# Performance work log

Measured on AMD Instinct MI355X. Metric: run time of the kernel, lower is better.

The kernel has to match this reference:

```python
import jax, jax.numpy as jnp
import numpy as np

N = 20000        # nodes
E = 160000       # directed edges (before self loops)
NODE_DIM = 1287
HEADS = 4
C1, C2, C3 = 128, 256, 128
ACT_SLOPE = 0.15   # module's LeakyReLU between layers
GAT_SLOPE = 0.2    # PyG GATConv default negative_slope


def _gat_layer(x, src, dst, W, att_src, att_dst, bias, heads, out_dim, concat):
    # x: [N, in] ; W: [in, heads*out] ; att_*: [heads, out] ; bias: [heads*out] or [out]
    h = (x @ W).reshape(N, heads, out_dim)                      # [N, H, C]
    a_s = jnp.einsum('nhc,hc->nh', h, att_src)                  # [N, H]
    a_d = jnp.einsum('nhc,hc->nh', h, att_dst)                  # [N, H]
    e = jax.nn.leaky_relu(a_s[src] + a_d[dst], GAT_SLOPE)       # [Etot, H]
    # segment softmax over incoming edges of each dst node (self loops => no empty segments)
    m = jax.ops.segment_max(e, dst, num_segments=N)             # [N, H]
    w = jnp.exp(e - m[dst])
    den = jax.ops.segment_sum(w, dst, num_segments=N)           # [N, H]
    alpha = w / den[dst]                                        # [Etot, H]
    msg = h[src] * alpha[:, :, None]                            # [Etot, H, C]
    out = jax.ops.segment_sum(msg, dst, num_segments=N)         # [N, H, C]
    out = out.reshape(N, heads * out_dim) if concat else out.mean(axis=1)
    return out + bias


def setup_inputs() -> dict:
    key = jax.random.key(0)
    ks = jax.random.split(key, 22)
    s = 0.05
    x = jax.random.normal(ks[0], (N, NODE_DIM), jnp.float32)
    edge_index = jax.random.randint(ks[1], (2, E), 0, N, dtype=jnp.int64)
    inp = {
        'x': x, 'edge_index': edge_index,
        'W1': jax.random.normal(ks[2], (NODE_DIM, HEADS * C1), jnp.float32) * s,
        'as1': jax.random.normal(ks[3], (HEADS, C1), jnp.float32) * s,
        'ad1': jax.random.normal(ks[4], (HEADS, C1), jnp.float32) * s,
        'b1': jnp.zeros((HEADS * C1,), jnp.float32),
        'W2': jax.random.normal(ks[5], (HEADS * C1, HEADS * C2), jnp.float32) * s,
        'as2': jax.random.normal(ks[6], (HEADS, C2), jnp.float32) * s,
        'ad2': jax.random.normal(ks[7], (HEADS, C2), jnp.float32) * s,
        'b2': jnp.zeros((HEADS * C2,), jnp.float32),
        # conv3: 1024 -> 128, 1 head, no concat
        'W3': jax.random.normal(ks[8], (HEADS * C2, C3), jnp.float32) * s,
        'as3': jax.random.normal(ks[9], (1, C3), jnp.float32) * s,
        'ad3': jax.random.normal(ks[10], (1, C3), jnp.float32) * s,
        'b3': jnp.zeros((C3,), jnp.float32),
        # pre_fc: 128 -> 16
        'pw': jax.random.normal(ks[11], (C3, 16), jnp.float32) * s,
        'pb': jnp.zeros((16,), jnp.float32),
        # fc fallback: Linear(16,32) -> LeakyReLU(0.15) -> Linear(32,2)
        'f1w': jax.random.normal(ks[12], (16, 32), jnp.float32) * s,
        'f1b': jnp.zeros((32,), jnp.float32),
        'f2w': jax.random.normal(ks[13], (32, 2), jnp.float32) * s,
        'f2b': jnp.zeros((2,), jnp.float32),
    }
    return inp


def reference(x, edge_index, W1, as1, ad1, b1, W2, as2, ad2, b2,
              W3, as3, ad3, b3, pw, pb, f1w, f1b, f2w, f2b):
    loop = jnp.arange(N, dtype=edge_index.dtype)
    src = jnp.concatenate([edge_index[0], loop])   # PyG add_self_loops=True
    dst = jnp.concatenate([edge_index[1], loop])
    h = _gat_layer(x, src, dst, W1, as1, ad1, b1, HEADS, C1, True)
    h = jax.nn.leaky_relu(h, ACT_SLOPE)            # dropout = identity (eval)
    h = _gat_layer(h, src, dst, W2, as2, ad2, b2, HEADS, C2, True)
    h = jax.nn.leaky_relu(h, ACT_SLOPE)
    h = _gat_layer(h, src, dst, W3, as3, ad3, b3, 1, C3, False)
    h = jax.nn.leaky_relu(h, ACT_SLOPE)
    h = h @ pw + pb                                 # pre_fc (128 -> 16)
    h = jax.nn.leaky_relu(h @ f1w + f1b, ACT_SLOPE)
    return h @ f2w + f2b                            # [N, 2] logits
```

## Files before the change

kernel.cpp:

```cpp
#include <hip/hip_runtime.h>
#include <hip/hip_bf16.h>
#include <cstdint>
#include <cstddef>

#define LRELU(x, s) ((x) > 0.f ? (x) : (s) * (x))

typedef __attribute__((ext_vector_type(8))) short bf16x8;
typedef __attribute__((ext_vector_type(4))) float f32x4;

__device__ __forceinline__ float bflo(uint v) { return __uint_as_float(v << 16); }
__device__ __forceinline__ float bfhi(uint v) { return __uint_as_float(v & 0xffff0000u); }
__device__ __forceinline__ ushort f2bf(float f) {
  const uint u = __float_as_uint(f);
  return (ushort)((u + 0x7fffu + ((u >> 16) & 1u)) >> 16);
}
__device__ __forceinline__ float rl_f(float x, int j) {
  return __uint_as_float(__builtin_amdgcn_readlane(__float_as_uint(x), j));
}

__device__ __forceinline__ void async16(const ushort* g, ushort* l) {
  __builtin_amdgcn_global_load_lds(
      (const __attribute__((address_space(1))) unsigned int*)g,
      (__attribute__((address_space(3))) unsigned int*)l, 16, 0, 0);
}

#define WAITCNT_VM(n) (0xF70 | (n))

__global__ void cast_pad_rows(const float* __restrict__ in, ushort* __restrict__ out,
                              int rows, int K, int Kp) {
  const int P4 = Kp >> 2;
  const long long idx = (long long)blockIdx.x * blockDim.x + threadIdx.x;
  if (idx >= (long long)rows * P4) return;
  const int r = (int)(idx / P4);
  const int c = ((int)(idx - (long long)r * P4)) << 2;
  const float* p = in + (size_t)r * K + c;
  float v0 = 0.f, v1 = 0.f, v2 = 0.f, v3 = 0.f;
  if (c + 3 < K) { v0 = p[0]; v1 = p[1]; v2 = p[2]; v3 = p[3]; }
  else {
    if (c + 0 < K) v0 = p[0];
    if (c + 1 < K) v1 = p[1];
    if (c + 2 < K) v2 = p[2];
    if (c + 3 < K) v3 = p[3];
  }
  uint2 o;
  o.x = (uint)f2bf(v0) | ((uint)f2bf(v1) << 16);
  o.y = (uint)f2bf(v2) | ((uint)f2bf(v3) << 16);
  *(uint2*)(out + (size_t)r * Kp + c) = o;
}

__global__ void cast_W_T(const float* __restrict__ W, ushort* __restrict__ Wt,
                         int K, int Nn, int Kp) {
  __shared__ float tile[32][33];
  const int kt = blockIdx.x * 32;
  const int nt = blockIdx.y * 32;
  const int tx = threadIdx.x;
  const int ty = threadIdx.y;
  for (int r = ty; r < 32; r += 8) {
    const int k = kt + r, nn = nt + tx;
    tile[r][tx] = (k < K && nn < Nn) ? W[(size_t)k * Nn + nn] : 0.f;
  }
  __syncthreads();
  for (int r = ty; r < 32; r += 8) {
    const int nn = nt + r, k = kt + tx;
    if (nn < Nn && k < Kp) Wt[(size_t)nn * Kp + k] = f2bf(tile[tx][r]);
  }
}

template <int TM, int TAG>
__global__ __launch_bounds__(256) void gemm_bf16(
    const ushort* __restrict__ A, const ushort* __restrict__ Bt, ushort* __restrict__ C,
    int M, int N, int Kp) {
  constexpr int MI = TM / 32;
  constexpr int LPG = (TM == 128) ? 4 : 3;
  __shared__ ushort sA[2 * TM * 32];
  __shared__ ushort sB[2 * 128 * 32];
  const int tid = threadIdx.x;
  const int wave = tid >> 6;
  const int lane = tid & 63;
  const int tilesN = N >> 7;
  const int nwg = gridDim.x;
  const int q8 = nwg >> 3, r8 = nwg & 7;
  const int xcd = blockIdx.x & 7;
  const int lid = blockIdx.x >> 3;
  const int wg = (xcd < r8 ? xcd * (q8 + 1) : r8 * (q8 + 1) + (xcd - r8) * q8) + lid;
  const int bx = wg % tilesN;
  const int by = wg / tilesN;
  const int wrow = (wave >> 1) * (TM / 2);
  const int wcol = (wave & 1) * 64;
  const int quad = lane >> 4;
  const int ml = lane & 15;

  const int seg = (((lane & 3) ^ ((lane >> 3) & 3)) * 8);
  const int rB0 = wave * 32 + (lane >> 2);
  const int gB0 = bx * 128 + rB0;
  const ushort* pB0 = Bt + (size_t)gB0 * Kp + seg;
  const ushort* pB1 = Bt + (size_t)(gB0 + 16) * Kp + seg;
  ushort* lB0 = &sB[(wave * 32) * 32];
  ushort* lB1 = &sB[(wave * 32 + 16) * 32];
  const ushort *pA0, *pA1;
  ushort *lA0, *lA1;
  if constexpr (TM == 128) {
    const int r0 = wave * 32 + (lane >> 2);
    pA0 = A + (size_t)min(by * TM + r0, M - 1) * Kp + seg;
    pA1 = A + (size_t)min(by * TM + r0 + 16, M - 1) * Kp + seg;
    lA0 = &sA[(wave * 32) * 32];
    lA1 = &sA[(wave * 32 + 16) * 32];
  } else {
    const int r0 = wave * 16 + (lane >> 2);
    pA0 = A + (size_t)min(by * TM + r0, M - 1) * Kp + seg;
    pA1 = nullptr;
    lA0 = &sA[(wave * 16) * 32];
    lA1 = nullptr;
  }

  const int nIter = Kp >> 5;
  auto issue = [&](int it, int p) {
    const int k0 = it << 5;
    const int oa = p * TM * 32;
    const int ob_ = p * 128 * 32;
    async16(pA0 + k0, lA0 + oa);
    if constexpr (TM == 128) async16(pA1 + k0, lA1 + oa);
    async16(pB0 + k0, lB0 + ob_);
    async16(pB1 + k0, lB1 + ob_);
  };

  f32x4 acc[MI][4];
#pragma unroll
  for (int mi = 0; mi < MI; mi++)
#pragma unroll
    for (int ni = 0; ni < 4; ni++)
#pragma unroll
      for (int e = 0; e < 4; e++) acc[mi][ni][e] = 0.f;

  const int rq = (quad ^ ((ml >> 1) & 3)) * 8;

  issue(0, 0);
  if (nIter > 1) issue(1, 1);
  int p = 0;
  for (int it = 0; it < nIter; ++it) {
    if (it + 1 < nIter) __builtin_amdgcn_s_waitcnt(WAITCNT_VM(LPG));
    else __builtin_amdgcn_s_waitcnt(WAITCNT_VM(0));
    __builtin_amdgcn_s_barrier();
    const ushort* bA = &sA[p * TM * 32];
    const ushort* bB = &sB[p * 128 * 32];
    bf16x8 af[MI], bfr[4];
#pragma unroll
    for (int mi = 0; mi < MI; mi++)
      af[mi] = *(const bf16x8*)&bA[(wrow + mi * 16 + ml) * 32 + rq];
#pragma unroll
    for (int ni = 0; ni < 4; ni++)
      bfr[ni] = *(const bf16x8*)&bB[(wcol + ni * 16 + ml) * 32 + rq];
#pragma unroll
    for (int mi = 0; mi < MI; mi++)
#pragma unroll
      for (int ni = 0; ni < 4; ni++)
        acc[mi][ni] = __builtin_amdgcn_mfma_f32_16x16x32_bf16(af[mi], bfr[ni], acc[mi][ni], 0, 0, 0);
    if (it + 2 < nIter) {
      __builtin_amdgcn_s_barrier();
      issue(it + 2, p);
    }
    p ^= 1;
  }

#pragma unroll
  for (int mi = 0; mi < MI; mi++) {
#pragma unroll
    for (int r = 0; r < 4; r++) {
      const int row = by * TM + wrow + mi * 16 + quad * 4 + r;
      if (row < M) {
#pragma unroll
        for (int ni = 0; ni < 4; ni++) {
          const int col = bx * 128 + wcol + ni * 16 + ml;
          C[(size_t)row * N + col] = f2bf(acc[mi][ni][r]);
        }
      }
    }
  }
}

template <int H, int C>
__global__ __launch_bounds__(256) void att_dots(
    const ushort* __restrict__ hb, const float* __restrict__ AS,
    const float* __restrict__ AD, float* __restrict__ asb, float* __restrict__ adb,
    int Nn) {
  constexpr int HC = H * C;
  constexpr int EPL = HC / 64;
  constexpr int S = C / EPL;
  const int n = blockIdx.x * 4 + (threadIdx.x >> 6);
  const int lane = threadIdx.x & 63;
  if (n >= Nn) return;
  const int head = lane / S;
  const int cbase = (lane % S) * EPL;
  const ushort* row = hb + (size_t)n * HC + lane * EPL;
  const float* as_h = AS + head * C;
  const float* ad_h = AD + head * C;
  float ps = 0.f, pd = 0.f;
#pragma unroll
  for (int j = 0; j < EPL; j += 2) {
    const uint v = *(const uint*)(row + j);
    const float lo = bflo(v), hi = bfhi(v);
    ps += lo * as_h[cbase + j] + hi * as_h[cbase + j + 1];
    pd += lo * ad_h[cbase + j] + hi * ad_h[cbase + j + 1];
  }
#pragma unroll
  for (int off = 1; off < S; off <<= 1) {
    ps += __shfl_xor(ps, off);
    pd += __shfl_xor(pd, off);
  }
  if ((lane % S) == 0) {
    asb[n * H + head] = ps;
    adb[n * H + head] = pd;
  }
}

__global__ void count_deg(const int* __restrict__ dst, int E, int* __restrict__ deg) {
  const int t = blockIdx.x * blockDim.x + threadIdx.x;
  if (t < E) atomicAdd(&deg[dst[t]], 1);
}

__global__ __launch_bounds__(1024) void scan_kernel(const int* __restrict__ deg,
                                                    int* __restrict__ rowptr,
                                                    int* __restrict__ cursor, int n) {
  __shared__ int swsum[16];
  __shared__ int carry_s;
  const int t = threadIdx.x;
  const int wv = t >> 6, lane = t & 63;
  if (t == 0) carry_s = 0;
  __syncthreads();
  for (int base = 0; base < n; base += 1024) {
    const int i = base + t;
    const int v = (i < n) ? (deg[i] + 1) : 0;
    int sc = v;
#pragma unroll
    for (int off = 1; off < 64; off <<= 1) {
      const int u = __shfl_up(sc, off);
      if (lane >= off) sc += u;
    }
    if (lane == 63) swsum[wv] = sc;
    __syncthreads();
    if (t < 16) {
      int x = swsum[t];
#pragma unroll
      for (int off = 1; off < 16; off <<= 1) {
        const int u = __shfl_up(x, off);
        if (t >= off) x += u;
      }
      swsum[t] = x;
    }
    __syncthreads();
    const int incl = sc + (wv == 0 ? 0 : swsum[wv - 1]) + carry_s;
    if (i < n) { rowptr[i + 1] = incl; cursor[i] = incl - v; }
    if (base == 0 && t == 0) rowptr[0] = 0;
    __syncthreads();
    if (t == 0) carry_s += swsum[15];
    __syncthreads();
  }
}

__global__ void scatter_edges(const int* __restrict__ esrc, const int* __restrict__ edst,
                              int E, int Etot, int* __restrict__ cursor,
                              int* __restrict__ csr_src) {
  const int t = blockIdx.x * blockDim.x + threadIdx.x;
  if (t >= Etot) return;
  int s, d;
  if (t < E) { s = esrc[t]; d = edst[t]; } else { s = t - E; d = s; }
  const int pos = atomicAdd(&cursor[d], 1);
  csr_src[pos] = s;
}

template <int H, int C>
__global__ __launch_bounds__(256) void gat_agg_wave(
    const ushort* __restrict__ hb, const int* __restrict__ rowptr,
    const int* __restrict__ csr_src, const float* __restrict__ a_s,
    const float* __restrict__ a_d, const float* __restrict__ bias,
    ushort* __restrict__ outb, float act_slope, int Nn) {
  constexpr int HC = H * C;
  constexpr int NU = HC / 2;
  constexpr int UPT = NU / 256;
  constexpr int GRP = (UPT == 2) ? 4 : 8;
  const int n = blockIdx.x * 4 + (threadIdx.x >> 6);
  const int lane = threadIdx.x & 63;
  if (n >= Nn) return;
  float ad_n[H];
#pragma unroll
  for (int h = 0; h < H; h++) ad_n[h] = a_d[n * H + h];
  const int start = rowptr[n], end = rowptr[n + 1];
  f32x4 acc[UPT][2];
#pragma unroll
  for (int q = 0; q < UPT; q++)
#pragma unroll
    for (int u = 0; u < 2; u++)
#pragma unroll
      for (int e = 0; e < 4; e++) acc[q][u][e] = 0.f;
  float den[H];
#pragma unroll
  for (int h = 0; h < H; h++) den[h] = 0.f;

  for (int base = start; base < end; base += 64) {
    const int cnt = min(64, end - base);
    int s = 0;
    float w[H];
#pragma unroll
    for (int h = 0; h < H; h++) w[h] = 0.f;
    if (lane < cnt) {
      s = csr_src[base + lane];
      float asv[H];
      if constexpr (H == 4) {
        const float4 t4 = *(const float4*)(a_s + s * 4);
        asv[0] = t4.x; asv[1] = t4.y; asv[2] = t4.z; asv[3] = t4.w;
      } else {
        asv[0] = a_s[s];
      }
#pragma unroll
      for (int h = 0; h < H; h++) {
        float lg = asv[h] + ad_n[h];
        lg = LRELU(lg, 0.2f);
        w[h] = __expf(lg);
        den[h] += w[h];
      }
    }
    const int cntg = cnt & ~(GRP - 1);
    int j = 0;
    for (; j < cntg; j += GRP) {
      uint4 v[GRP][UPT];
#pragma unroll
      for (int g = 0; g < GRP; g++) {
        const int sj = __builtin_amdgcn_readlane(s, j + g);
        const uint4* hp = (const uint4*)(hb + (size_t)sj * HC);
#pragma unroll
        for (int q = 0; q < UPT; q++) v[g][q] = hp[q * 64 + lane];
      }
#pragma unroll
      for (int g = 0; g < GRP; g++) {
        float wj[H];
#pragma unroll
        for (int h = 0; h < H; h++) wj[h] = rl_f(w[h], j + g);
#pragma unroll
        for (int q = 0; q < UPT; q++) {
          const int e0 = q * 512 + 8 * lane;
          const float wq = wj[e0 / C];
          acc[q][0][0] += wq * bflo(v[g][q].x);
          acc[q][0][1] += wq * bfhi(v[g][q].x);
          acc[q][0][2] += wq * bflo(v[g][q].y);
          acc[q][0][3] += wq * bfhi(v[g][q].y);
          acc[q][1][0] += wq * bflo(v[g][q].z);
          acc[q][1][1] += wq * bfhi(v[g][q].z);
          acc[q][1][2] += wq * bflo(v[g][q].w);
          acc[q][1][3] += wq * bfhi(v[g][q].w);
        }
      }
    }
    for (; j < cnt; j++) {
      const int sj = __builtin_amdgcn_readlane(s, j);
      float wj[H];
#pragma unroll
      for (int h = 0; h < H; h++) wj[h] = rl_f(w[h], j);
      const uint4* hp = (const uint4*)(hb + (size_t)sj * HC);
#pragma unroll
      for (int q = 0; q < UPT; q++) {
        const int e0 = q * 512 + 8 * lane;
        const uint4 v = hp[q * 64 + lane];
        const float wq = wj[e0 / C];
        acc[q][0][0] += wq * bflo(v.x);
        acc[q][0][1] += wq * bfhi(v.x);
        acc[q][0][2] += wq * bflo(v.y);
        acc[q][0][3] += wq * bfhi(v.y);
        acc[q][1][0] += wq * bflo(v.z);
        acc[q][1][1] += wq * bfhi(v.z);
        acc[q][1][2] += wq * bflo(v.w);
        acc[q][1][3] += wq * bfhi(v.w);
      }
    }
  }
#pragma unroll
  for (int h = 0; h < H; h++) {
#pragma unroll
    for (int off = 1; off < 64; off <<= 1) den[h] += __shfl_xor(den[h], off);
    den[h] = 1.f / den[h];
  }
#pragma unroll
  for (int q = 0; q < UPT; q++) {
    const int e0 = q * 512 + 8 * lane;
    const float iv = den[e0 / C];
    const float4 ba = *(const float4*)(bias + e0);
    const float4 bb = *(const float4*)(bias + e0 + 4);
    const float o0 = LRELU(acc[q][0][0] * iv + ba.x, act_slope);
    const float o1 = LRELU(acc[q][0][1] * iv + ba.y, act_slope);
    const float o2 = LRELU(acc[q][0][2] * iv + ba.z, act_slope);
    const float o3 = LRELU(acc[q][0][3] * iv + ba.w, act_slope);
    const float o4 = LRELU(acc[q][1][0] * iv + bb.x, act_slope);
    const float o5 = LRELU(acc[q][1][1] * iv + bb.y, act_slope);
    const float o6 = LRELU(acc[q][1][2] * iv + bb.z, act_slope);
    const float o7 = LRELU(acc[q][1][3] * iv + bb.w, act_slope);
    uint4 o;
    o.x = (uint)f2bf(o0) | ((uint)f2bf(o1) << 16);
    o.y = (uint)f2bf(o2) | ((uint)f2bf(o3) << 16);
    o.z = (uint)f2bf(o4) | ((uint)f2bf(o5) << 16);
    o.w = (uint)f2bf(o6) | ((uint)f2bf(o7) << 16);
    ((uint4*)outb)[(size_t)n * (NU / 4) + q * 64 + lane] = o;
  }
}

__global__ __launch_bounds__(64) void gat_agg3_mlp(
    const ushort* __restrict__ hb, const int* __restrict__ rowptr,
    const int* __restrict__ csr_src, const float* __restrict__ a_s,
    const float* __restrict__ a_d, const float* __restrict__ b3,
    const float* __restrict__ pw, const float* __restrict__ pb,
    const float* __restrict__ f1w, const float* __restrict__ f1b,
    const float* __restrict__ f2w, const float* __restrict__ f2b,
    float* __restrict__ out) {
  const int n = blockIdx.x;
  const int tid = threadIdx.x;
  __shared__ float sx[128];
  __shared__ float s1[16];
  __shared__ float s2[32];
  const float ad_n = a_d[n];
  const int start = rowptr[n], end = rowptr[n + 1];
  float2 acc = make_float2(0.f, 0.f);
  float den = 0.f;
  for (int base = start; base < end; base += 64) {
    const int cnt = min(64, end - base);
    int s = 0;
    float w = 0.f;
    if (tid < cnt) {
      s = csr_src[base + tid];
      float lg = a_s[s] + ad_n;
      lg = LRELU(lg, 0.2f);
      w = __expf(lg);
      den += w;
    }
    const int cntg = cnt & ~7;
    int j = 0;
    for (; j < cntg; j += 8) {
      uint v[8];
      float wj[8];
#pragma unroll
      for (int g = 0; g < 8; g++) {
        const int sj = __builtin_amdgcn_readlane(s, j + g);
        v[g] = ((const uint*)(hb + (size_t)sj * 128))[tid];
        wj[g] = rl_f(w, j + g);
      }
#pragma unroll
      for (int g = 0; g < 8; g++) {
        acc.x += wj[g] * bflo(v[g]);
        acc.y += wj[g] * bfhi(v[g]);
      }
    }
    for (; j < cnt; j++) {
      const int sj = __builtin_amdgcn_readlane(s, j);
      const float wj = rl_f(w, j);
      const uint v = ((const uint*)(hb + (size_t)sj * 128))[tid];
      acc.x += wj * bflo(v);
      acc.y += wj * bfhi(v);
    }
  }
#pragma unroll
  for (int off = 1; off < 64; off <<= 1) den += __shfl_xor(den, off);
  const float iv = 1.f / den;
  sx[2 * tid]     = LRELU(acc.x * iv + b3[2 * tid], 0.15f);
  sx[2 * tid + 1] = LRELU(acc.y * iv + b3[2 * tid + 1], 0.15f);
  __syncthreads();
  if (tid < 16) {
    float a = pb[tid];
    for (int c = 0; c < 128; c++) a += sx[c] * pw[c * 16 + tid];
    s1[tid] = a;
  }
  __syncthreads();
  if (tid < 32) {
    float a = f1b[tid];
    for (int c = 0; c < 16; c++) a += s1[c] * f1w[c * 32 + tid];
    s2[tid] = LRELU(a, 0.15f);
  }
  __syncthreads();
  if (tid < 2) {
    float a = f2b[tid];
    for (int c = 0; c < 32; c++) a += s2[c] * f2w[c * 2 + tid];
    out[(size_t)n * 2 + tid] = a;
  }
}

extern "C" void kernel_launch(void* const* d_in, const int* in_sizes, int n_in,
                              void* d_out, int out_size, void* d_ws, size_t ws_size,
                              hipStream_t stream) {
  const float* x   = (const float*)d_in[0];
  const int* ei    = (const int*)d_in[1];
  const float* W1  = (const float*)d_in[2];
  const float* as1 = (const float*)d_in[3];
  const float* ad1 = (const float*)d_in[4];
  const float* b1  = (const float*)d_in[5];
  const float* W2  = (const float*)d_in[6];
  const float* as2 = (const float*)d_in[7];
  const float* ad2 = (const float*)d_in[8];
  const float* b2  = (const float*)d_in[9];
  const float* W3  = (const float*)d_in[10];
  const float* as3 = (const float*)d_in[11];
  const float* ad3 = (const float*)d_in[12];
  const float* b3  = (const float*)d_in[13];
  const float* pw  = (const float*)d_in[14];
  const float* pb  = (const float*)d_in[15];
  const float* f1w = (const float*)d_in[16];
  const float* f1b = (const float*)d_in[17];
  const float* f2w = (const float*)d_in[18];
  const float* f2b = (const float*)d_in[19];
  float* out = (float*)d_out;

  const int N = in_sizes[0] / 1287;
  const int E = in_sizes[1] / 2;
  const int Etot = E + N;
  const int* esrc = ei;
  const int* edst = ei + E;
  const int K1 = 1287, K1p = 1312;

  char* ws = (char*)d_ws;
  size_t off = 0;
  auto alloc = [&](size_t bytes) -> void* {
    void* p = ws + off;
    off = (off + bytes + 255) & ~(size_t)255;
    return p;
  };
  ushort* hb  = (ushort*)alloc((size_t)N * 1024 * 2);
  ushort* ob  = (ushort*)alloc((size_t)N * 1024 * 2);
  ushort* xb  = (ushort*)alloc((size_t)N * K1p * 2);
  ushort* W1t = (ushort*)alloc((size_t)512 * K1p * 2);
  ushort* W2t = (ushort*)alloc((size_t)1024 * 512 * 2);
  ushort* W3t = (ushort*)alloc((size_t)128 * 1024 * 2);
  float* av   = (float*)alloc((size_t)N * 8 * sizeof(float));
  int* deg    = (int*)alloc((size_t)N * sizeof(int));
  int* rowptr = (int*)alloc((size_t)(N + 1) * sizeof(int));
  int* cursor = (int*)alloc((size_t)N * sizeof(int));
  int* csr    = (int*)alloc((size_t)Etot * sizeof(int));
  float* asb = av;
  float* adb = av + (size_t)N * 4;

  hipMemsetAsync(deg, 0, (size_t)N * sizeof(int), stream);
  count_deg<<<(E + 255) / 256, 256, 0, stream>>>(edst, E, deg);
  scan_kernel<<<1, 1024, 0, stream>>>(deg, rowptr, cursor, N);
  scatter_edges<<<(Etot + 255) / 256, 256, 0, stream>>>(esrc, edst, E, Etot, cursor, csr);

  {
    const long long nx = (long long)N * (K1p / 4);
    cast_pad_rows<<<(int)((nx + 255) / 256), 256, 0, stream>>>(x, xb, N, K1, K1p);
    cast_W_T<<<dim3(K1p / 32, (512 + 31) / 32), dim3(32, 8), 0, stream>>>(W1, W1t, K1, 512, K1p);
    cast_W_T<<<dim3(512 / 32, 1024 / 32), dim3(32, 8), 0, stream>>>(W2, W2t, 512, 1024, 512);
    cast_W_T<<<dim3(1024 / 32, 128 / 32), dim3(32, 8), 0, stream>>>(W3, W3t, 1024, 128, 1024);
  }

  const int tilesM = (N + 127) / 128;
  const int tilesM64 = (N + 63) / 64;
  const int nodeBlocks = (N + 3) / 4;

  {
    const int HC = 512;
    gemm_bf16<128, 1><<<tilesM * (HC / 128), 256, 0, stream>>>(xb, W1t, hb, N, HC, K1p);
    att_dots<4, 128><<<nodeBlocks, 256, 0, stream>>>(hb, as1, ad1, asb, adb, N);
    gat_agg_wave<4, 128><<<nodeBlocks, 256, 0, stream>>>(hb, rowptr, csr, asb, adb,
                                                         b1, ob, 0.15f, N);
  }
  {
    const int HC = 1024;
    gemm_bf16<128, 2><<<tilesM * (HC / 128), 256, 0, stream>>>(ob, W2t, hb, N, HC, 512);
    att_dots<4, 256><<<nodeBlocks, 256, 0, stream>>>(hb, as2, ad2, asb, adb, N);
    gat_agg_wave<4, 256><<<nodeBlocks, 256, 0, stream>>>(hb, rowptr, csr, asb, adb,
                                                         b2, ob, 0.15f, N);
  }
  {
    const int HC = 128;
    gemm_bf16<64, 3><<<tilesM64 * (HC / 128), 256, 0, stream>>>(ob, W3t, hb, N, HC, 1024);
    att_dots<1, 128><<<nodeBlocks, 256, 0, stream>>>(hb, as3, ad3, asb, adb, N);
    gat_agg3_mlp<<<N, 64, 0, stream>>>(hb, rowptr, csr, asb, adb, b3,
                                       pw, pb, f1w, f1b, f2w, f2b, out);
  }
}
```

Baseline: 479.5 us.

## Fuse prep kernels, triple-buffer GEMM loads, batch layer-3 aggregation per wave

Merges the x cast, the three weight transposes and the degree memset into one `prep_all` launch, replacing several launches and a memset. The bf16 GEMM moves from double to triple LDS buffering, so the next-but-one tile load is issued right after the single barrier. This drops the second barrier per K step, at the cost of more shared memory per block. The final aggregation+MLP kernel now handles four nodes per 256-thread block, one per wave, and computes the small MLP with lane-parallel partial dots and shuffle reductions instead of serial single-thread loops and block barriers.

Result: faster. 455.4 us (-5.0%).

```diff
diff --git a/kernel.cpp b/kernel.cpp
--- a/kernel.cpp
+++ b/kernel.cpp
@@ -26,35 +26,51 @@
 
 #define WAITCNT_VM(n) (0xF70 | (n))
 
-__global__ void cast_pad_rows(const float* __restrict__ in, ushort* __restrict__ out,
-                              int rows, int K, int Kp) {
-  const int P4 = Kp >> 2;
-  const long long idx = (long long)blockIdx.x * blockDim.x + threadIdx.x;
-  if (idx >= (long long)rows * P4) return;
-  const int r = (int)(idx / P4);
-  const int c = ((int)(idx - (long long)r * P4)) << 2;
-  const float* p = in + (size_t)r * K + c;
-  float v0 = 0.f, v1 = 0.f, v2 = 0.f, v3 = 0.f;
-  if (c + 3 < K) { v0 = p[0]; v1 = p[1]; v2 = p[2]; v3 = p[3]; }
+__global__ __launch_bounds__(256) void prep_all(
+    const float* __restrict__ x, ushort* __restrict__ xb,
+    const float* __restrict__ W1, ushort* __restrict__ W1t,
+    const float* __restrict__ W2, ushort* __restrict__ W2t,
+    const float* __restrict__ W3, ushort* __restrict__ W3t,
+    int* __restrict__ deg,
+    int N, int K1, int K1p, int nA, int nB, int nC, int nD) {
+  __shared__ float tile[32][33];
+  const int tid = threadIdx.x;
+  int b = blockIdx.x;
+  if (b < nA) {
+    const int P4 = K1p >> 2;
+    const long long idx = (long long)b * 256 + tid;
+    if (idx < (long long)N * P4) {
+      const int r = (int)(idx / P4);
+      const int c = ((int)(idx - (long long)r * P4)) << 2;
+      const float* p = x + (size_t)r * K1 + c;
+      float v0 = 0.f, v1 = 0.f, v2 = 0.f, v3 = 0.f;
+      if (c + 3 < K1) { v0 = p[0]; v1 = p[1]; v2 = p[2]; v3 = p[3]; }
+      else {
+        if (c + 0 < K1) v0 = p[0];
+        if (c + 1 < K1) v1 = p[1];
+        if (c + 2 < K1) v2 = p[2];
+        if (c + 3 < K1) v3 = p[3];
+      }
+      uint2 o;
+      o.x = (uint)f2bf(v0) | ((uint)f2bf(v1) << 16);
+      o.y = (uint)f2bf(v2) | ((uint)f2bf(v3) << 16);
+      *(uint2*)(xb + (size_t)r * K1p + c) = o;
+    }
+    return;
+  }
+  b -= nA;
+  const float* W; ushort* Wt; int K, Nn, Kp, tilesK;
+  if (b < nB)           { W = W1; Wt = W1t; K = K1;   Nn = 512;  Kp = K1p;  tilesK = K1p / 32; }
+  else if (b < nB + nC) { b -= nB; W = W2; Wt = W2t; K = 512;  Nn = 1024; Kp = 512;  tilesK = 16; }
+  else if (b < nB + nC + nD) { b -= nB + nC; W = W3; Wt = W3t; K = 1024; Nn = 128; Kp = 1024; tilesK = 32; }
   else {
-    if (c + 0 < K) v0 = p[0];
-    if (c + 1 < K) v1 = p[1];
-    if (c + 2 < K) v2 = p[2];
-    if (c + 3 < K) v3 = p[3];
-  }
-  uint2 o;
-  o.x = (uint)f2bf(v0) | ((uint)f2bf(v1) << 16);
-  o.y = (uint)f2bf(v2) | ((uint)f2bf(v3) << 16);
-  *(uint2*)(out + (size_t)r * Kp + c) = o;
-}
-
-__global__ void cast_W_T(const float* __restrict__ W, ushort* __restrict__ Wt,
-                         int K, int Nn, int Kp) {
-  __shared__ float tile[32][33];
-  const int kt = blockIdx.x * 32;
-  const int nt = blockIdx.y * 32;
-  const int tx = threadIdx.x;
-  const int ty = threadIdx.y;
+    const int i = (b - nB - nC - nD) * 256 + tid;
+    if (i < N) deg[i] = 0;
+    return;
+  }
+  const int kt = (b % tilesK) * 32;
+  const int nt = (b / tilesK) * 32;
+  const int tx = tid & 31, ty = tid >> 5;
   for (int r = ty; r < 32; r += 8) {
     const int k = kt + r, nn = nt + tx;
     tile[r][tx] = (k < K && nn < Nn) ? W[(size_t)k * Nn + nn] : 0.f;
@@ -72,8 +88,8 @@
     int M, int N, int Kp) {
   constexpr int MI = TM / 32;
   constexpr int LPG = (TM == 128) ? 4 : 3;
-  __shared__ ushort sA[2 * TM * 32];
-  __shared__ ushort sB[2 * 128 * 32];
+  __shared__ ushort sA[3 * TM * 32];
+  __shared__ ushort sB[3 * 128 * 32];
   const int tid = threadIdx.x;
   const int wave = tid >> 6;
   const int lane = tid & 63;
@@ -136,13 +152,17 @@
 
   issue(0, 0);
   if (nIter > 1) issue(1, 1);
-  int p = 0;
+  int b = 0;
   for (int it = 0; it < nIter; ++it) {
     if (it + 1 < nIter) __builtin_amdgcn_s_waitcnt(WAITCNT_VM(LPG));
     else __builtin_amdgcn_s_waitcnt(WAITCNT_VM(0));
     __builtin_amdgcn_s_barrier();
-    const ushort* bA = &sA[p * TM * 32];
-    const ushort* bB = &sB[p * 128 * 32];
+    if (it + 2 < nIter) {
+      const int b2 = (b + 2 >= 3) ? b - 1 : b + 2;
+      issue(it + 2, b2);
+    }
+    const ushort* bA = &sA[b * TM * 32];
+    const ushort* bB = &sB[b * 128 * 32];
     bf16x8 af[MI], bfr[4];
 #pragma unroll
     for (int mi = 0; mi < MI; mi++)
@@ -155,11 +175,7 @@
 #pragma unroll
       for (int ni = 0; ni < 4; ni++)
         acc[mi][ni] = __builtin_amdgcn_mfma_f32_16x16x32_bf16(af[mi], bfr[ni], acc[mi][ni], 0, 0, 0);
-    if (it + 2 < nIter) {
-      __builtin_amdgcn_s_barrier();
-      issue(it + 2, p);
-    }
-    p ^= 1;
+    b = (b + 1 == 3) ? 0 : b + 1;
   }
 
 #pragma unroll
@@ -401,19 +417,21 @@
   }
 }
 
-__global__ __launch_bounds__(64) void gat_agg3_mlp(
+__global__ __launch_bounds__(256) void gat_agg3_mlp(
     const ushort* __restrict__ hb, const int* __restrict__ rowptr,
     const int* __restrict__ csr_src, const float* __restrict__ a_s,
     const float* __restrict__ a_d, const float* __restrict__ b3,
     const float* __restrict__ pw, const float* __restrict__ pb,
     const float* __restrict__ f1w, const float* __restrict__ f1b,
     const float* __restrict__ f2w, const float* __restrict__ f2b,
-    float* __restrict__ out) {
-  const int n = blockIdx.x;
-  const int tid = threadIdx.x;
-  __shared__ float sx[128];
-  __shared__ float s1[16];
-  __shared__ float s2[32];
+    float* __restrict__ out, int Nn) {
+  __shared__ float sx[4][128];
+  __shared__ float s1[4][16];
+  __shared__ float s2[4][32];
+  const int w = threadIdx.x >> 6;
+  const int lane = threadIdx.x & 63;
+  const int n = blockIdx.x * 4 + w;
+  if (n >= Nn) return;
   const float ad_n = a_d[n];
   const int start = rowptr[n], end = rowptr[n + 1];
   float2 acc = make_float2(0.f, 0.f);
@@ -421,13 +439,13 @@
   for (int base = start; base < end; base += 64) {
     const int cnt = min(64, end - base);
     int s = 0;
-    float w = 0.f;
-    if (tid < cnt) {
-      s = csr_src[base + tid];
+    float wv_ = 0.f;
+    if (lane < cnt) {
+      s = csr_src[base + lane];
       float lg = a_s[s] + ad_n;
       lg = LRELU(lg, 0.2f);
-      w = __expf(lg);
-      den += w;
+      wv_ = __expf(lg);
+      den += wv_;
     }
     const int cntg = cnt & ~7;
     int j = 0;
@@ -437,8 +455,8 @@
 #pragma unroll
       for (int g = 0; g < 8; g++) {
         const int sj = __builtin_amdgcn_readlane(s, j + g);
-        v[g] = ((const uint*)(hb + (size_t)sj * 128))[tid];
-        wj[g] = rl_f(w, j + g);
+        v[g] = ((const uint*)(hb + (size_t)sj * 128))[lane];
+        wj[g] = rl_f(wv_, j + g);
       }
 #pragma unroll
       for (int g = 0; g < 8; g++) {
@@ -448,8 +466,8 @@
     }
     for (; j < cnt; j++) {
       const int sj = __builtin_amdgcn_readlane(s, j);
-      const float wj = rl_f(w, j);
-      const uint v = ((const uint*)(hb + (size_t)sj * 128))[tid];
+      const float wj = rl_f(wv_, j);
+      const uint v = ((const uint*)(hb + (size_t)sj * 128))[lane];
       acc.x += wj * bflo(v);
       acc.y += wj * bfhi(v);
     }
@@ -457,25 +475,34 @@
 #pragma unroll
   for (int off = 1; off < 64; off <<= 1) den += __shfl_xor(den, off);
   const float iv = 1.f / den;
-  sx[2 * tid]     = LRELU(acc.x * iv + b3[2 * tid], 0.15f);
-  sx[2 * tid + 1] = LRELU(acc.y * iv + b3[2 * tid + 1], 0.15f);
-  __syncthreads();
-  if (tid < 16) {
-    float a = pb[tid];
-    for (int c = 0; c < 128; c++) a += sx[c] * pw[c * 16 + tid];
-    s1[tid] = a;
-  }
-  __syncthreads();
-  if (tid < 32) {
-    float a = f1b[tid];
-    for (int c = 0; c < 16; c++) a += s1[c] * f1w[c * 32 + tid];
-    s2[tid] = LRELU(a, 0.15f);
-  }
-  __syncthreads();
-  if (tid < 2) {
-    float a = f2b[tid];
-    for (int c = 0; c < 32; c++) a += s2[c] * f2w[c * 2 + tid];
-    out[(size_t)n * 2 + tid] = a;
+  sx[w][2 * lane]     = LRELU(acc.x * iv + b3[2 * lane], 0.15f);
+  sx[w][2 * lane + 1] = LRELU(acc.y * iv + b3[2 * lane + 1], 0.15f);
+  {
+    const int o = lane & 15, p = lane >> 4;
+    float a = 0.f;
+#pragma unroll
+    for (int c = 0; c < 32; c++) a += sx[w][p * 32 + c] * pw[(p * 32 + c) * 16 + o];
+    a += __shfl_xor(a, 16);
+    a += __shfl_xor(a, 32);
+    if (lane < 16) s1[w][o] = a + pb[o];
+  }
+  {
+    const int o = lane & 31, p = lane >> 5;
+    float a = 0.f;
+#pragma unroll
+    for (int c = 0; c < 8; c++) a += s1[w][p * 8 + c] * f1w[(p * 8 + c) * 32 + o];
+    a += __shfl_xor(a, 32);
+    if (lane < 32) s2[w][o] = LRELU(a + f1b[o], 0.15f);
+  }
+  {
+    const int o = lane & 1, p = lane >> 1;
+    float a = s2[w][p] * f2w[p * 2 + o];
+    a += __shfl_xor(a, 2);
+    a += __shfl_xor(a, 4);
+    a += __shfl_xor(a, 8);
+    a += __shfl_xor(a, 16);
+    a += __shfl_xor(a, 32);
+    if (lane < 2) out[(size_t)n * 2 + o] = a + f2b[o];
   }
 }
 
@@ -532,18 +559,17 @@
   float* asb = av;
   float* adb = av + (size_t)N * 4;
 
-  hipMemsetAsync(deg, 0, (size_t)N * sizeof(int), stream);
+  const int nA = (int)(((long long)N * (K1p / 4) + 255) / 256);
+  const int nB = (K1p / 32) * (512 / 32);
+  const int nC = (512 / 32) * (1024 / 32);
+  const int nD = (1024 / 32) * (128 / 32);
+  const int nE = (N + 255) / 256;
+  prep_all<<<nA + nB + nC + nD + nE, 256, 0, stream>>>(
+      x, xb, W1, W1t, W2, W2t, W3, W3t, deg, N, K1, K1p, nA, nB, nC, nD);
+
   count_deg<<<(E + 255) / 256, 256, 0, stream>>>(edst, E, deg);
   scan_kernel<<<1, 1024, 0, stream>>>(deg, rowptr, cursor, N);
   scatter_edges<<<(Etot + 255) / 256, 256, 0, stream>>>(esrc, edst, E, Etot, cursor, csr);
-
-  {
-    const long long nx = (long long)N * (K1p / 4);
-    cast_pad_rows<<<(int)((nx + 255) / 256), 256, 0, stream>>>(x, xb, N, K1, K1p);
-    cast_W_T<<<dim3(K1p / 32, (512 + 31) / 32), dim3(32, 8), 0, stream>>>(W1, W1t, K1, 512, K1p);
-    cast_W_T<<<dim3(512 / 32, 1024 / 32), dim3(32, 8), 0, stream>>>(W2, W2t, 512, 1024, 512);
-    cast_W_T<<<dim3(1024 / 32, 128 / 32), dim3(32, 8), 0, stream>>>(W3, W3t, 1024, 128, 1024);
-  }
 
   const int tilesM = (N + 127) / 128;
   const int tilesM64 = (N + 63) / 64;
@@ -567,7 +593,7 @@
     const int HC = 128;
     gemm_bf16<64, 3><<<tilesM64 * (HC / 128), 256, 0, stream>>>(ob, W3t, hb, N, HC, 1024);
     att_dots<1, 128><<<nodeBlocks, 256, 0, stream>>>(hb, as3, ad3, asb, adb, N);
-    gat_agg3_mlp<<<N, 64, 0, stream>>>(hb, rowptr, csr, asb, adb, b3,
-                                       pw, pb, f1w, f1b, f2w, f2b, out);
-  }
-}
+    gat_agg3_mlp<<<nodeBlocks, 256, 0, stream>>>(hb, rowptr, csr, asb, adb, b3,
+                                                 pw, pb, f1w, f1b, f2w, f2b, out, N);
+  }
+}
```
